# Kernel optimization log

Measured on AMD Instinct MI355X. Metric: run time of the kernel, lower is better.

Reference implementation:

```python
import jax, jax.numpy as jnp
import numpy as np

N, L, IN_DIM, H, E = 16, 4096, 32, 1, 512
D = H * E  # d_model
FF = E     # feed_forward_dimensions = embed_dim
EPS_ATTN = 1e-6
EPS_LN = 1e-5


def _ln(x, g, b):
    mu = jnp.mean(x, axis=-1, keepdims=True)
    var = jnp.mean(jnp.square(x - mu), axis=-1, keepdims=True)
    return (x - mu) * jax.lax.rsqrt(var + EPS_LN) * g + b


def setup_inputs() -> dict:
    key = jax.random.key(0)
    ks = jax.random.split(key, 16)
    s = 0.02
    inp = {
        "x": jax.random.normal(ks[0], (N, L, IN_DIM), dtype=jnp.float32),
        "w_in": jax.random.normal(ks[1], (D, IN_DIM), dtype=jnp.float32) * s,
        "b_in": jnp.zeros((D,), jnp.float32),
        "wq": jax.random.normal(ks[2], (H * E, D), dtype=jnp.float32) * s,
        "bq": jnp.zeros((H * E,), jnp.float32),
        "wk": jax.random.normal(ks[3], (H * E, D), dtype=jnp.float32) * s,
        "bk": jnp.zeros((H * E,), jnp.float32),
        "wv": jax.random.normal(ks[4], (H * E, D), dtype=jnp.float32) * s,
        "bv": jnp.zeros((H * E,), jnp.float32),
        "wo": jax.random.normal(ks[5], (D, H * E), dtype=jnp.float32) * s,
        "bo": jnp.zeros((D,), jnp.float32),
        "g1": jnp.ones((D,), jnp.float32),
        "b1": jnp.zeros((D,), jnp.float32),
        "w_ff1": jax.random.normal(ks[6], (FF, D), dtype=jnp.float32) * s,
        "b_ff1": jnp.zeros((FF,), jnp.float32),
        "w_ff2": jax.random.normal(ks[7], (D, FF), dtype=jnp.float32) * s,
        "b_ff2": jnp.zeros((D,), jnp.float32),
        "g2": jnp.ones((D,), jnp.float32),
        "b2": jnp.zeros((D,), jnp.float32),
        "gf": jnp.ones((D,), jnp.float32),
        "bf": jnp.zeros((D,), jnp.float32),
        "w_fc": jax.random.normal(ks[8], (1, D), dtype=jnp.float32) * s,
        "b_fc": jnp.zeros((1,), jnp.float32),
    }
    return inp


def reference(x, w_in, b_in, wq, bq, wk, bk, wv, bv, wo, bo, g1, b1,
              w_ff1, b_ff1, w_ff2, b_ff2, g2, b2, gf, bf, w_fc, b_fc):
    # input projection
    h = x @ w_in.T + b_in  # [N,L,D]
    # attention layer: q/k/v projections, split heads
    q = (h @ wq.T + bq).reshape(N, L, H, E)
    k = (h @ wk.T + bk).reshape(N, L, H, E)
    v = (h @ wv.T + bv).reshape(N, L, H, E)
    # linear attention: elu+1 feature map, non-causal aggregation
    Q = jax.nn.elu(q) + 1.0
    K = jax.nn.elu(k) + 1.0
    KV = jnp.einsum("nshd,nshm->nhdm", K, v)          # [N,H,E,E]
    Z = 1.0 / (jnp.einsum("nlhd,nhd->nlh", Q, K.sum(axis=1)) + EPS_ATTN)
    attn = jnp.einsum("nlhd,nhdm,nlh->nlhm", Q, KV, Z)  # [N,L,H,E]
    attn = attn.reshape(N, L, H * E) @ wo.T + bo
    # post-norm transformer encoder layer (dropout=0)
    h = _ln(h + attn, g1, b1)
    y = jax.nn.relu(h @ w_ff1.T + b_ff1) @ w_ff2.T + b_ff2
    h = _ln(h + y, g2, b2)
    # final encoder normalization
    h = _ln(h, gf, bf)
    out = h @ w_fc.T + b_fc  # [N,L,1]
    return out[:, 0, 0]
```

## Files before the change

### kernel.cpp

```cpp
#include <hip/hip_runtime.h>
#include <hip/hip_bf16.h>

typedef unsigned short u16;
typedef __attribute__((ext_vector_type(8))) unsigned short ushort8;
typedef __attribute__((ext_vector_type(8))) __bf16 bf16x8;
typedef __attribute__((ext_vector_type(4))) float f32x4;

#define NB 16
#define SEQ 4096
#define DIM 512
#define INDIM 32
#define NTOK (NB * SEQ)
#define WBM 128
#define NTILE (NTOK / WBM)

static __device__ __forceinline__ u16 f2bf(float f) {
    union { float f; unsigned u; } x; x.f = f;
    unsigned r = (x.u + 0x7FFFu + ((x.u >> 16) & 1u)) >> 16;
    return (u16)r;
}
static __device__ __forceinline__ float bf2f(u16 b) {
    union { unsigned u; float f; } x; x.u = ((unsigned)b) << 16;
    return x.f;
}

__device__ __forceinline__ float dot32(const float* __restrict__ w, const float* v) {
    const float4* a = (const float4*)w;
    float acc = 0.f;
    #pragma unroll
    for (int i = 0; i < 8; ++i) {
        float4 p = a[i];
        acc += p.x * v[4*i] + p.y * v[4*i+1] + p.z * v[4*i+2] + p.w * v[4*i+3];
    }
    return acc;
}

__global__ __launch_bounds__(256) void k_p1(
    const float* __restrict__ wq, const float* __restrict__ wk, const float* __restrict__ wv,
    const float* __restrict__ wo, const float* __restrict__ w_in, const float* __restrict__ b_in,
    const float* __restrict__ bq, const float* __restrict__ bk, const float* __restrict__ bv,
    const float* __restrict__ bo, const float* __restrict__ g1, const float* __restrict__ b1,
    const float* __restrict__ wff1, const float* __restrict__ wff2,
    float* __restrict__ wq2, float* __restrict__ bq2,
    u16* __restrict__ wk2b, float* __restrict__ bk2,
    float* __restrict__ wv2, float* __restrict__ wvb,
    float* __restrict__ wf1x, float* __restrict__ wf1c,
    float* __restrict__ wg1, float* __restrict__ wb1, float* __restrict__ bb,
    u16* __restrict__ woT, u16* __restrict__ wff1g1T, u16* __restrict__ wff2T) {
    __shared__ float smem[64 * 65];
    int bid = blockIdx.x, tid = threadIdx.x;

    if (bid < 1536) {
        int mat = bid >> 9, e = bid & 511;
        int kc = tid >> 5, j = tid & 31;
        const float* A = (mat == 0 ? wq : (mat == 1 ? wk : wv)) + (long)e * DIM;
        float acc = 0.f, accb = 0.f;
        int d0 = kc * 64;
        #pragma unroll 8
        for (int i = 0; i < 64; ++i) {
            float a = A[d0 + i];
            acc  += a * w_in[(d0 + i) * INDIM + j];
            accb += a * b_in[d0 + i];
        }
        float* sA = smem;
        float* sS = smem + 256;
        sA[kc * 32 + j] = acc;
        if (j == 0) sS[kc] = accb;
        __syncthreads();
        if (tid < 32) {
            float s = 0.f;
            #pragma unroll
            for (int i = 0; i < 8; ++i) s += sA[i * 32 + tid];
            if (mat == 0) wq2[e * INDIM + tid] = s;
            else if (mat == 1) wk2b[e * INDIM + tid] = f2bf(s);
            else wv2[e * INDIM + tid] = s;
        } else if (tid == 32) {
            float s = 0.f;
            #pragma unroll
            for (int i = 0; i < 8; ++i) s += sS[i];
            if (mat == 0) bq2[e] = bq[e] + s;
            else if (mat == 1) bk2[e] = bk[e] + s;
            else wvb[e] = s + bv[e];
        }
    } else if (bid < 2048) {
        int e = bid - 1536;
        int kc = tid >> 5, j = tid & 31;
        const float* A = wff1 + (long)e * DIM;
        float accx = 0.f, accc = 0.f, accg = 0.f, accb1 = 0.f;
        int d0 = kc * 64;
        #pragma unroll 4
        for (int i = 0; i < 64; ++i) {
            int d = d0 + i;
            float a = A[d], g = g1[d], ag = a * g;
            accx  += ag * w_in[d * INDIM + j];
            accc  += ag * (b_in[d] + bo[d]);
            accg  += ag;
            accb1 += a * b1[d];
        }
        float* sA = smem;
        float* s0 = smem + 256;
        float* s1p = smem + 264;
        float* s2 = smem + 272;
        sA[kc * 32 + j] = accx;
        if (j == 0) { s0[kc] = accc; s1p[kc] = accg; s2[kc] = accb1; }
        __syncthreads();
        if (tid < 32) {
            float s = 0.f;
            #pragma unroll
            for (int i = 0; i < 8; ++i) s += sA[i * 32 + tid];
            wf1x[e * INDIM + tid] = s;
        } else if (tid == 32) {
            float s = 0.f;
            #pragma unroll
            for (int i = 0; i < 8; ++i) s += s0[i];
            wf1c[e] = s;
        } else if (tid == 33) {
            float s = 0.f;
            #pragma unroll
            for (int i = 0; i < 8; ++i) s += s1p[i];
            wg1[e] = s;
        } else if (tid == 34) {
            float s = 0.f;
            #pragma unroll
            for (int i = 0; i < 8; ++i) s += s2[i];
            wb1[e] = s;
        } else if (tid == 35) {
            bb[e] = b_in[e] + bo[e];
        }
    } else {
        int t = bid - 2048;
        int m = t >> 6;
        int tt = t & 63;
        int r = tt >> 3, c = tt & 7;
        const float* M = (m == 0) ? wo : (m == 1 ? wff1 : wff2);
        u16* MT = (m == 0) ? woT : (m == 1 ? wff1g1T : wff2T);
        float* tile = smem;
        int rr = tid >> 2, cc = (tid & 3) * 16;
        const float* src = M + (long)(r * 64 + rr) * DIM + c * 64 + cc;
        #pragma unroll
        for (int i = 0; i < 4; ++i) {
            float4 v = *(const float4*)(src + i * 4);
            tile[rr * 65 + cc + i * 4 + 0] = v.x;
            tile[rr * 65 + cc + i * 4 + 1] = v.y;
            tile[rr * 65 + cc + i * 4 + 2] = v.z;
            tile[rr * 65 + cc + i * 4 + 3] = v.w;
        }
        __syncthreads();
        int orr = tid >> 2, occ = (tid & 3) * 16;
        float gk = (m == 1) ? g1[c * 64 + orr] : 1.f;
        u16 ob[16];
        #pragma unroll
        for (int i = 0; i < 16; ++i) ob[i] = f2bf(tile[(occ + i) * 65 + orr] * gk);
        u16* dst = MT + (long)(c * 64 + orr) * DIM + r * 64 + occ;
        *(ushort8*)dst = *(ushort8*)ob;
        *(ushort8*)(dst + 8) = *(ushort8*)(ob + 8);
    }
}

__global__ __launch_bounds__(256) void k_w(
    const float* __restrict__ x,
    const float* __restrict__ wq2, const float* __restrict__ bq2,
    const u16* __restrict__ wk2b, const float* __restrict__ bk2,
    float* __restrict__ xup, float* __restrict__ zdp) {
    __shared__ u16 sB[DIM * 40];
    __shared__ float s_q0[DIM];
    __shared__ float sw[WBM];
    __shared__ float sxu8[8][32];
    __shared__ float szz[8];
    __shared__ float sx0[INDIM];
    int tid = threadIdx.x;
    int tt = blockIdx.x;
    int lane = tid & 63, wid = tid >> 6;
    long tbase = (long)tt * WBM;
    int batch = (int)(tbase >> 12);

    #pragma unroll
    for (int pp = 0; pp < 8; ++pp) {
        int f = (pp * 256 + tid) * 8;
        int row = f >> 5, colc = f & 31;
        ushort8 v = *(const ushort8*)(wk2b + f);
        *(ushort8*)(sB + row * 40 + colc) = v;
    }
    if (tid < INDIM) sx0[tid] = x[(long)batch * SEQ * INDIM + tid];
    __syncthreads();
    #pragma unroll
    for (int rep = 0; rep < 2; ++rep) {
        int e = tid + rep * 256;
        float a = bq2[e] + dot32(wq2 + e * INDIM, sx0);
        s_q0[e] = (a > 0.f) ? (a + 1.f) : __expf(a);
    }

    int col = lane & 15;
    int koff = (lane >> 4) * 8;
    bf16x8 fa[2];
    #pragma unroll
    for (int mi = 0; mi < 2; ++mi) {
        const float* xr = x + (tbase + wid * 32 + mi * 16 + col) * INDIM + koff;
        float4 a0 = *(const float4*)(xr);
        float4 a1 = *(const float4*)(xr + 4);
        u16 tmp[8] = { f2bf(a0.x), f2bf(a0.y), f2bf(a0.z), f2bf(a0.w),
                       f2bf(a1.x), f2bf(a1.y), f2bf(a1.z), f2bf(a1.w) };
        fa[mi] = *(bf16x8*)tmp;
    }
    __syncthreads();

    float q0v[32], bkv[32];
    #pragma unroll
    for (int ni = 0; ni < 32; ++ni) {
        q0v[ni] = s_q0[ni * 16 + col];
        bkv[ni] = bk2[ni * 16 + col];
    }

    f32x4 zero = {0.f, 0.f, 0.f, 0.f};
    float wpart[2][4] = {};
    #pragma unroll
    for (int nc = 0; nc < 4; ++nc) {
        bf16x8 fb[8];
        #pragma unroll
        for (int nj = 0; nj < 8; ++nj) {
            int row = (nc * 8 + nj) * 16 + col;
            fb[nj] = *(const bf16x8*)(sB + row * 40 + koff);
        }
        #pragma unroll
        for (int mi = 0; mi < 2; ++mi) {
            #pragma unroll
            for (int nj = 0; nj < 8; ++nj) {
                f32x4 acc = __builtin_amdgcn_mfma_f32_16x16x32_bf16(fa[mi], fb[nj], zero, 0, 0, 0);
                int ni = nc * 8 + nj;
                #pragma unroll
                for (int r = 0; r < 4; ++r) {
                    float v = acc[r] + bkv[ni];
                    v = (v > 0.f) ? (v + 1.f) : __expf(v);
                    wpart[mi][r] += v * q0v[ni];
                }
            }
        }
    }
    #pragma unroll
    for (int mi = 0; mi < 2; ++mi) {
        #pragma unroll
        for (int r = 0; r < 4; ++r) {
            float s = wpart[mi][r];
            s += __shfl_xor(s, 1, 64); s += __shfl_xor(s, 2, 64);
            s += __shfl_xor(s, 4, 64); s += __shfl_xor(s, 8, 64);
            if (col == 0) sw[wid * 32 + mi * 16 + (lane >> 4) * 4 + r] = s;
        }
    }
    __syncthreads();
    {
        int j = tid & 31, g = tid >> 5;
        float a = 0.f, z = 0.f;
        for (int tl = g; tl < WBM; tl += 8) {
            float wv_ = sw[tl];
            a += wv_ * x[(tbase + tl) * INDIM + j];
            if (j == 0) z += wv_;
        }
        sxu8[g][j] = a;
        if (j == 0) szz[g] = z;
    }
    __syncthreads();
    if (tid < 32) {
        float a = 0.f;
        #pragma unroll
        for (int g = 0; g < 8; ++g) a += sxu8[g][tid];
        xup[tt * INDIM + tid] = a;
    } else if (tid == 32) {
        float z = 0.f;
        #pragma unroll
        for (int g = 0; g < 8; ++g) z += szz[g];
        zdp[tt] = z;
    }
}

__device__ __forceinline__ void reduce2_512(float a, float b, int tid, float* l16,
                                            float& oa, float& ob) {
    #pragma unroll
    for (int off = 1; off < 64; off <<= 1) {
        a += __shfl_xor(a, off, 64);
        b += __shfl_xor(b, off, 64);
    }
    int w = tid >> 6;
    if ((tid & 63) == 0) { l16[w] = a; l16[8 + w] = b; }
    __syncthreads();
    float ra = 0.f, rb = 0.f;
    #pragma unroll
    for (int i = 0; i < 8; ++i) { ra += l16[i]; rb += l16[8 + i]; }
    oa = ra; ob = rb;
    __syncthreads();
}

__device__ __forceinline__ float gemv512(const u16* __restrict__ MT,
                                         const float* __restrict__ vec,
                                         float* __restrict__ spart,
                                         int tid, int d) {
    int kc = tid >> 6, dg = tid & 63;
    float ps[8] = {};
    const u16* base = MT + (long)(kc * 64) * DIM + dg * 8;
    #pragma unroll 8
    for (int k8 = 0; k8 < 64; ++k8) {
        ushort8 w8 = *(const ushort8*)(base + (long)k8 * DIM);
        float fk = vec[kc * 64 + k8];
        #pragma unroll
        for (int j = 0; j < 8; ++j) ps[j] += bf2f(w8[j]) * fk;
    }
    #pragma unroll
    for (int j = 0; j < 8; ++j) spart[kc * DIM + dg * 8 + j] = ps[j];
    __syncthreads();
    float acc = 0.f;
    #pragma unroll
    for (int i = 0; i < 8; ++i) acc += spart[i * DIM + d];
    return acc;
}

__global__ __launch_bounds__(512) void k_final(
    const float* __restrict__ x, const float* __restrict__ w_in,
    const float* __restrict__ wv2, const float* __restrict__ wvb,
    const float* __restrict__ bb,
    const float* __restrict__ wf1x, const float* __restrict__ wf1c,
    const float* __restrict__ wg1, const float* __restrict__ wb1,
    const float* __restrict__ g1, const float* __restrict__ b1,
    const float* __restrict__ bff1, const float* __restrict__ bff2,
    const u16* __restrict__ woT, const u16* __restrict__ wff1g1T,
    const u16* __restrict__ wff2T,
    const float* __restrict__ g2, const float* __restrict__ b2,
    const float* __restrict__ gf, const float* __restrict__ bfv,
    const float* __restrict__ wfc, const float* __restrict__ bfc,
    const float* __restrict__ xup, const float* __restrict__ zdp,
    float* __restrict__ out) {
    __shared__ float sx0[INDIM], sxu[INDIM];
    __shared__ float sv[DIM];
    __shared__ float sf[DIM];
    __shared__ float spart[8 * DIM];
    __shared__ float l16[16];
    __shared__ float szd;
    int n = blockIdx.x, tid = threadIdx.x, d = tid;
    if (tid < INDIM) {
        float a = 0.f;
        #pragma unroll 8
        for (int slot = 0; slot < 32; ++slot)
            a += xup[(n * 32 + slot) * INDIM + tid];
        sxu[tid] = a;
        sx0[tid] = x[(long)n * SEQ * INDIM + tid];
    } else if (tid == 32) {
        float z = 0.f;
        #pragma unroll 8
        for (int slot = 0; slot < 32; ++slot) z += zdp[n * 32 + slot];
        szd = z;
    }
    __syncthreads();
    float zd = szd;
    float Z = 1.f / (zd + 1e-6f);
    float zz = zd * Z;

    float u2d = dot32(wv2 + d * INDIM, sxu);
    sv[d] = Z * u2d + zz * wvb[d];
    __syncthreads();

    float o_d = gemv512(woT, sv, spart, tid, d);

    float rd = bb[d] + dot32(w_in + d * INDIM, sx0) + o_d;
    sv[d] = o_d;
    float sum, sumsq;
    reduce2_512(rd, rd * rd, tid, l16, sum, sumsq);
    float mu1 = sum * (1.f / DIM);
    float s1 = rsqrtf(sumsq * (1.f / DIM) - mu1 * mu1 + 1e-5f);
    float r1 = (rd - mu1) * s1 * g1[d] + b1[d];

    float W_d = gemv512(wff1g1T, sv, spart, tid, d);
    float G = dot32(wf1x + d * INDIM, sx0) + W_d + wf1c[d];
    float fp = s1 * (G - mu1 * wg1[d]) + wb1[d] + bff1[d];
    __syncthreads();
    sf[d] = fmaxf(fp, 0.f);
    __syncthreads();

    float yacc = gemv512(wff2T, sf, spart, tid, d);
    float y = r1 + bff2[d] + yacc;

    reduce2_512(y, y * y, tid, l16, sum, sumsq);
    float mu2 = sum * (1.f / DIM);
    float inv2 = rsqrtf(sumsq * (1.f / DIM) - mu2 * mu2 + 1e-5f);
    float h2 = (y - mu2) * inv2 * g2[d] + b2[d];

    reduce2_512(h2, h2 * h2, tid, l16, sum, sumsq);
    float mu3 = sum * (1.f / DIM);
    float inv3 = rsqrtf(sumsq * (1.f / DIM) - mu3 * mu3 + 1e-5f);
    float h3 = (h2 - mu3) * inv3 * gf[d] + bfv[d];

    float pfc = wfc[d] * h3;
    float dummy;
    reduce2_512(pfc, 0.f, tid, l16, sum, dummy);
    if (tid == 0) out[n] = sum + bfc[0];
}

extern "C" void kernel_launch(void* const* d_in, const int* in_sizes, int n_in,
                              void* d_out, int out_size, void* d_ws, size_t ws_size,
                              hipStream_t stream) {
    const float* x    = (const float*)d_in[0];
    const float* w_in = (const float*)d_in[1];
    const float* b_in = (const float*)d_in[2];
    const float* wq   = (const float*)d_in[3];
    const float* bq   = (const float*)d_in[4];
    const float* wk   = (const float*)d_in[5];
    const float* bk   = (const float*)d_in[6];
    const float* wv   = (const float*)d_in[7];
    const float* bv   = (const float*)d_in[8];
    const float* wo   = (const float*)d_in[9];
    const float* bo   = (const float*)d_in[10];
    const float* g1   = (const float*)d_in[11];
    const float* b1   = (const float*)d_in[12];
    const float* wff1 = (const float*)d_in[13];
    const float* bff1 = (const float*)d_in[14];
    const float* wff2 = (const float*)d_in[15];
    const float* bff2 = (const float*)d_in[16];
    const float* g2   = (const float*)d_in[17];
    const float* b2   = (const float*)d_in[18];
    const float* gf   = (const float*)d_in[19];
    const float* bf   = (const float*)d_in[20];
    const float* wfc  = (const float*)d_in[21];
    const float* bfc  = (const float*)d_in[22];

    char* ws = (char*)d_ws;
    float* wq2     = (float*)(ws + 0);
    float* bq2     = (float*)(ws + 65536);
    u16*   wk2b    = (u16*)  (ws + 67584);
    float* bk2     = (float*)(ws + 100352);
    float* wv2     = (float*)(ws + 102400);
    float* wvb     = (float*)(ws + 167936);
    float* bb      = (float*)(ws + 169984);
    float* wf1x    = (float*)(ws + 172032);
    float* wf1c    = (float*)(ws + 237568);
    float* wg1     = (float*)(ws + 239616);
    float* wb1     = (float*)(ws + 241664);
    u16*   woT     = (u16*)  (ws + 243712);
    u16*   wff1g1T = (u16*)  (ws + 767872);
    u16*   wff2T   = (u16*)  (ws + 1292160);
    float* xup     = (float*)(ws + 1816448);
    float* zdp     = (float*)(ws + 1881984);

    k_p1<<<2240, 256, 0, stream>>>(wq, wk, wv, wo, w_in, b_in, bq, bk, bv, bo,
                                   g1, b1, wff1, wff2,
                                   wq2, bq2, wk2b, bk2, wv2, wvb,
                                   wf1x, wf1c, wg1, wb1, bb,
                                   woT, wff1g1T, wff2T);
    k_w<<<NTILE, 256, 0, stream>>>(x, wq2, bq2, wk2b, bk2, xup, zdp);
    k_final<<<NB, 512, 0, stream>>>(x, w_in, wv2, wvb, bb, wf1x, wf1c, wg1, wb1,
                                    g1, b1, bff1, bff2, woT, wff1g1T, wff2T,
                                    g2, b2, gf, bf, wfc, bfc, xup, zdp,
                                    (float*)d_out);
}
```

Measured before the change: 71.32 us.

## Fuse final per-batch epilogue into tile kernel via last-block atomic ticket

```diff
diff --git a/kernel.cpp b/kernel.cpp
--- a/kernel.cpp
+++ b/kernel.cpp
@@ -35,32 +35,43 @@
     return acc;
 }
 
-__global__ __launch_bounds__(256) void k_p1(
-    const float* __restrict__ wq, const float* __restrict__ wk, const float* __restrict__ wv,
-    const float* __restrict__ wo, const float* __restrict__ w_in, const float* __restrict__ b_in,
-    const float* __restrict__ bq, const float* __restrict__ bk, const float* __restrict__ bv,
-    const float* __restrict__ bo, const float* __restrict__ g1, const float* __restrict__ b1,
-    const float* __restrict__ wff1, const float* __restrict__ wff2,
-    float* __restrict__ wq2, float* __restrict__ bq2,
-    u16* __restrict__ wk2b, float* __restrict__ bk2,
-    float* __restrict__ wv2, float* __restrict__ wvb,
-    float* __restrict__ wf1x, float* __restrict__ wf1c,
-    float* __restrict__ wg1, float* __restrict__ wb1, float* __restrict__ bb,
-    u16* __restrict__ woT, u16* __restrict__ wff1g1T, u16* __restrict__ wff2T) {
+__device__ __forceinline__ float dot512(const float* __restrict__ w, const float* v) {
+    const float4* a = (const float4*)w;
+    float acc = 0.f;
+    #pragma unroll 4
+    for (int j = 0; j < 128; ++j) {
+        float4 p = a[j];
+        acc += p.x * v[4*j] + p.y * v[4*j+1] + p.z * v[4*j+2] + p.w * v[4*j+3];
+    }
+    return acc;
+}
+
+struct P {
+    const float *x, *w_in, *b_in, *wq, *bq, *wk, *bk, *wv, *bv, *wo, *bo;
+    const float *g1, *b1, *wff1, *bff1, *wff2, *bff2, *g2, *b2, *gf, *bfv, *wfc, *bfc;
+    u16 *wk2b; float *bk2, *wv2, *wvb;
+    float *bb, *wf1x, *wf1c, *wg1, *wb1;
+    u16 *woT, *wff1g1T, *wff2T;
+    float *q0, *xup, *zdp;
+    int *cnt;
+    float *out;
+};
+
+__global__ __launch_bounds__(256) void k_p1(P p) {
     __shared__ float smem[64 * 65];
     int bid = blockIdx.x, tid = threadIdx.x;
 
-    if (bid < 1536) {
+    if (bid < 1024) {
         int mat = bid >> 9, e = bid & 511;
         int kc = tid >> 5, j = tid & 31;
-        const float* A = (mat == 0 ? wq : (mat == 1 ? wk : wv)) + (long)e * DIM;
+        const float* A = (mat == 0 ? p.wk : p.wv) + (long)e * DIM;
         float acc = 0.f, accb = 0.f;
         int d0 = kc * 64;
         #pragma unroll 8
         for (int i = 0; i < 64; ++i) {
             float a = A[d0 + i];
-            acc  += a * w_in[(d0 + i) * INDIM + j];
-            accb += a * b_in[d0 + i];
+            acc  += a * p.w_in[(d0 + i) * INDIM + j];
+            accb += a * p.b_in[d0 + i];
         }
         float* sA = smem;
         float* sS = smem + 256;
@@ -71,31 +82,29 @@
             float s = 0.f;
             #pragma unroll
             for (int i = 0; i < 8; ++i) s += sA[i * 32 + tid];
-            if (mat == 0) wq2[e * INDIM + tid] = s;
-            else if (mat == 1) wk2b[e * INDIM + tid] = f2bf(s);
-            else wv2[e * INDIM + tid] = s;
+            if (mat == 0) p.wk2b[e * INDIM + tid] = f2bf(s);
+            else p.wv2[e * INDIM + tid] = s;
         } else if (tid == 32) {
             float s = 0.f;
             #pragma unroll
             for (int i = 0; i < 8; ++i) s += sS[i];
-            if (mat == 0) bq2[e] = bq[e] + s;
-            else if (mat == 1) bk2[e] = bk[e] + s;
-            else wvb[e] = s + bv[e];
-        }
-    } else if (bid < 2048) {
-        int e = bid - 1536;
+            if (mat == 0) p.bk2[e] = p.bk[e] + s;
+            else p.wvb[e] = s + p.bv[e];
+        }
+    } else if (bid < 1536) {
+        int e = bid - 1024;
         int kc = tid >> 5, j = tid & 31;
-        const float* A = wff1 + (long)e * DIM;
+        const float* A = p.wff1 + (long)e * DIM;
         float accx = 0.f, accc = 0.f, accg = 0.f, accb1 = 0.f;
         int d0 = kc * 64;
         #pragma unroll 4
         for (int i = 0; i < 64; ++i) {
             int d = d0 + i;
-            float a = A[d], g = g1[d], ag = a * g;
-            accx  += ag * w_in[d * INDIM + j];
-            accc  += ag * (b_in[d] + bo[d]);
+            float a = A[d], g = p.g1[d], ag = a * g;
+            accx  += ag * p.w_in[d * INDIM + j];
+            accc  += ag * (p.b_in[d] + p.bo[d]);
             accg  += ag;
-            accb1 += a * b1[d];
+            accb1 += a * p.b1[d];
         }
         float* sA = smem;
         float* s0 = smem + 256;
@@ -108,32 +117,32 @@
             float s = 0.f;
             #pragma unroll
             for (int i = 0; i < 8; ++i) s += sA[i * 32 + tid];
-            wf1x[e * INDIM + tid] = s;
+            p.wf1x[e * INDIM + tid] = s;
         } else if (tid == 32) {
             float s = 0.f;
             #pragma unroll
             for (int i = 0; i < 8; ++i) s += s0[i];
-            wf1c[e] = s;
+            p.wf1c[e] = s;
         } else if (tid == 33) {
             float s = 0.f;
             #pragma unroll
             for (int i = 0; i < 8; ++i) s += s1p[i];
-            wg1[e] = s;
+            p.wg1[e] = s;
         } else if (tid == 34) {
             float s = 0.f;
             #pragma unroll
             for (int i = 0; i < 8; ++i) s += s2[i];
-            wb1[e] = s;
+            p.wb1[e] = s;
         } else if (tid == 35) {
-            bb[e] = b_in[e] + bo[e];
-        }
-    } else {
-        int t = bid - 2048;
+            p.bb[e] = p.b_in[e] + p.bo[e];
+        }
+    } else if (bid < 1728) {
+        int t = bid - 1536;
         int m = t >> 6;
         int tt = t & 63;
         int r = tt >> 3, c = tt & 7;
-        const float* M = (m == 0) ? wo : (m == 1 ? wff1 : wff2);
-        u16* MT = (m == 0) ? woT : (m == 1 ? wff1g1T : wff2T);
+        const float* M = (m == 0) ? p.wo : (m == 1 ? p.wff1 : p.wff2);
+        u16* MT = (m == 0) ? p.woT : (m == 1 ? p.wff1g1T : p.wff2T);
         float* tile = smem;
         int rr = tid >> 2, cc = (tid & 3) * 16;
         const float* src = M + (long)(r * 64 + rr) * DIM + c * 64 + cc;
@@ -147,47 +156,175 @@
         }
         __syncthreads();
         int orr = tid >> 2, occ = (tid & 3) * 16;
-        float gk = (m == 1) ? g1[c * 64 + orr] : 1.f;
+        float gk = (m == 1) ? p.g1[c * 64 + orr] : 1.f;
         u16 ob[16];
         #pragma unroll
         for (int i = 0; i < 16; ++i) ob[i] = f2bf(tile[(occ + i) * 65 + orr] * gk);
         u16* dst = MT + (long)(c * 64 + orr) * DIM + r * 64 + occ;
         *(ushort8*)dst = *(ushort8*)ob;
         *(ushort8*)(dst + 8) = *(ushort8*)(ob + 8);
-    }
-}
-
-__global__ __launch_bounds__(256) void k_w(
-    const float* __restrict__ x,
-    const float* __restrict__ wq2, const float* __restrict__ bq2,
-    const u16* __restrict__ wk2b, const float* __restrict__ bk2,
-    float* __restrict__ xup, float* __restrict__ zdp) {
-    __shared__ u16 sB[DIM * 40];
-    __shared__ float s_q0[DIM];
-    __shared__ float sw[WBM];
-    __shared__ float sxu8[8][32];
-    __shared__ float szz[8];
-    __shared__ float sx0[INDIM];
+    } else {
+        int n = bid - 1728;
+        float* sx0 = smem;
+        float* sh = smem + 32;
+        if (tid < INDIM) sx0[tid] = p.x[(long)n * SEQ * INDIM + tid];
+        __syncthreads();
+        #pragma unroll
+        for (int rep = 0; rep < 2; ++rep) {
+            int d = tid + rep * 256;
+            sh[d] = p.b_in[d] + dot32(p.w_in + (long)d * INDIM, sx0);
+        }
+        __syncthreads();
+        #pragma unroll
+        for (int rep = 0; rep < 2; ++rep) {
+            int e = tid + rep * 256;
+            float a = p.bq[e] + dot512(p.wq + (long)e * DIM, sh);
+            p.q0[n * DIM + e] = (a > 0.f) ? (a + 1.f) : __expf(a);
+        }
+        if (tid == 0) p.cnt[n] = 0;
+    }
+}
+
+__device__ __forceinline__ void reduce2_256(float a, float b, int tid, float* l16,
+                                            float& oa, float& ob) {
+    #pragma unroll
+    for (int off = 1; off < 64; off <<= 1) {
+        a += __shfl_xor(a, off, 64);
+        b += __shfl_xor(b, off, 64);
+    }
+    int w = tid >> 6;
+    if ((tid & 63) == 0) { l16[w] = a; l16[4 + w] = b; }
+    __syncthreads();
+    oa = l16[0] + l16[1] + l16[2] + l16[3];
+    ob = l16[4] + l16[5] + l16[6] + l16[7];
+    __syncthreads();
+}
+
+__device__ __forceinline__ void gemv256(const u16* __restrict__ MT,
+                                        const float* __restrict__ vec,
+                                        float* __restrict__ spart,
+                                        int tid, float& o0, float& o1) {
+    int kc = tid >> 6, dg = tid & 63;
+    float ps[8] = {};
+    const u16* base = MT + (long)(kc * 128) * DIM + dg * 8;
+    #pragma unroll 8
+    for (int k8 = 0; k8 < 128; ++k8) {
+        ushort8 w8 = *(const ushort8*)(base + (long)k8 * DIM);
+        float fk = vec[kc * 128 + k8];
+        #pragma unroll
+        for (int j = 0; j < 8; ++j) ps[j] += bf2f(w8[j]) * fk;
+    }
+    #pragma unroll
+    for (int j = 0; j < 8; ++j) spart[kc * DIM + dg * 8 + j] = ps[j];
+    __syncthreads();
+    float a0 = 0.f, a1 = 0.f;
+    #pragma unroll
+    for (int i = 0; i < 4; ++i) {
+        a0 += spart[i * DIM + tid];
+        a1 += spart[i * DIM + tid + 256];
+    }
+    o0 = a0; o1 = a1;
+}
+
+__device__ void phaseE256(const P& p, int n, int tid, char* smem) {
+    float* sx0 = (float*)smem;
+    float* sxu = sx0 + 32;
+    float* sv  = sxu + 32;
+    float* sf  = sv + 512;
+    float* spart = sf + 512;
+    float* l16 = spart + 2048;
+    float* szd = l16 + 8;
+    if (tid < INDIM) {
+        float a = 0.f;
+        #pragma unroll 8
+        for (int slot = 0; slot < 32; ++slot)
+            a += p.xup[(n * 32 + slot) * INDIM + tid];
+        sxu[tid] = a;
+        sx0[tid] = p.x[(long)n * SEQ * INDIM + tid];
+    } else if (tid == 32) {
+        float z = 0.f;
+        #pragma unroll 8
+        for (int slot = 0; slot < 32; ++slot) z += p.zdp[n * 32 + slot];
+        szd[0] = z;
+    }
+    __syncthreads();
+    float zd = szd[0];
+    float Z = 1.f / (zd + 1e-6f);
+    float zz = zd * Z;
+    int d0 = tid, d1 = tid + 256;
+
+    sv[d0] = Z * dot32(p.wv2 + (long)d0 * INDIM, sxu) + zz * p.wvb[d0];
+    sv[d1] = Z * dot32(p.wv2 + (long)d1 * INDIM, sxu) + zz * p.wvb[d1];
+    __syncthreads();
+
+    float o0, o1;
+    gemv256(p.woT, sv, spart, tid, o0, o1);
+
+    float rd0 = p.bb[d0] + dot32(p.w_in + (long)d0 * INDIM, sx0) + o0;
+    float rd1 = p.bb[d1] + dot32(p.w_in + (long)d1 * INDIM, sx0) + o1;
+    sv[d0] = o0;
+    sv[d1] = o1;
+    float sum, sumsq;
+    reduce2_256(rd0 + rd1, rd0 * rd0 + rd1 * rd1, tid, l16, sum, sumsq);
+    float mu1 = sum * (1.f / DIM);
+    float s1 = rsqrtf(sumsq * (1.f / DIM) - mu1 * mu1 + 1e-5f);
+    float r1_0 = (rd0 - mu1) * s1 * p.g1[d0] + p.b1[d0];
+    float r1_1 = (rd1 - mu1) * s1 * p.g1[d1] + p.b1[d1];
+
+    float W0, W1;
+    gemv256(p.wff1g1T, sv, spart, tid, W0, W1);
+    float G0 = dot32(p.wf1x + (long)d0 * INDIM, sx0) + W0 + p.wf1c[d0];
+    float G1 = dot32(p.wf1x + (long)d1 * INDIM, sx0) + W1 + p.wf1c[d1];
+    float fp0 = s1 * (G0 - mu1 * p.wg1[d0]) + p.wb1[d0] + p.bff1[d0];
+    float fp1 = s1 * (G1 - mu1 * p.wg1[d1]) + p.wb1[d1] + p.bff1[d1];
+    __syncthreads();
+    sf[d0] = fmaxf(fp0, 0.f);
+    sf[d1] = fmaxf(fp1, 0.f);
+    __syncthreads();
+
+    float ya0, ya1;
+    gemv256(p.wff2T, sf, spart, tid, ya0, ya1);
+    float y0 = r1_0 + p.bff2[d0] + ya0;
+    float y1 = r1_1 + p.bff2[d1] + ya1;
+
+    reduce2_256(y0 + y1, y0 * y0 + y1 * y1, tid, l16, sum, sumsq);
+    float mu2 = sum * (1.f / DIM);
+    float inv2 = rsqrtf(sumsq * (1.f / DIM) - mu2 * mu2 + 1e-5f);
+    float h2_0 = (y0 - mu2) * inv2 * p.g2[d0] + p.b2[d0];
+    float h2_1 = (y1 - mu2) * inv2 * p.g2[d1] + p.b2[d1];
+
+    reduce2_256(h2_0 + h2_1, h2_0 * h2_0 + h2_1 * h2_1, tid, l16, sum, sumsq);
+    float mu3 = sum * (1.f / DIM);
+    float inv3 = rsqrtf(sumsq * (1.f / DIM) - mu3 * mu3 + 1e-5f);
+    float h3_0 = (h2_0 - mu3) * inv3 * p.gf[d0] + p.bfv[d0];
+    float h3_1 = (h2_1 - mu3) * inv3 * p.gf[d1] + p.bfv[d1];
+
+    float pr = p.wfc[d0] * h3_0 + p.wfc[d1] * h3_1;
+    float dummy;
+    reduce2_256(pr, 0.f, tid, l16, sum, dummy);
+    if (tid == 0) p.out[n] = sum + p.bfc[0];
+}
+
+__global__ __launch_bounds__(256) void k_wE(P p) {
+    __shared__ __align__(16) char smem[45056];
+    __shared__ int sTicket;
     int tid = threadIdx.x;
     int tt = blockIdx.x;
     int lane = tid & 63, wid = tid >> 6;
     long tbase = (long)tt * WBM;
     int batch = (int)(tbase >> 12);
 
+    u16* sB = (u16*)smem;
+    float* sw = (float*)(smem + 40960);
+    float* sxu8 = (float*)(smem + 41472);
+    float* szz = (float*)(smem + 42496);
+
     #pragma unroll
     for (int pp = 0; pp < 8; ++pp) {
         int f = (pp * 256 + tid) * 8;
         int row = f >> 5, colc = f & 31;
-        ushort8 v = *(const ushort8*)(wk2b + f);
+        ushort8 v = *(const ushort8*)(p.wk2b + f);
         *(ushort8*)(sB + row * 40 + colc) = v;
-    }
-    if (tid < INDIM) sx0[tid] = x[(long)batch * SEQ * INDIM + tid];
-    __syncthreads();
-    #pragma unroll
-    for (int rep = 0; rep < 2; ++rep) {
-        int e = tid + rep * 256;
-        float a = bq2[e] + dot32(wq2 + e * INDIM, sx0);
-        s_q0[e] = (a > 0.f) ? (a + 1.f) : __expf(a);
     }
 
     int col = lane & 15;
@@ -195,21 +332,20 @@
     bf16x8 fa[2];
     #pragma unroll
     for (int mi = 0; mi < 2; ++mi) {
-        const float* xr = x + (tbase + wid * 32 + mi * 16 + col) * INDIM + koff;
+        const float* xr = p.x + (tbase + wid * 32 + mi * 16 + col) * INDIM + koff;
         float4 a0 = *(const float4*)(xr);
         float4 a1 = *(const float4*)(xr + 4);
         u16 tmp[8] = { f2bf(a0.x), f2bf(a0.y), f2bf(a0.z), f2bf(a0.w),
                        f2bf(a1.x), f2bf(a1.y), f2bf(a1.z), f2bf(a1.w) };
         fa[mi] = *(bf16x8*)tmp;
     }
-    __syncthreads();
-
     float q0v[32], bkv[32];
     #pragma unroll
     for (int ni = 0; ni < 32; ++ni) {
-        q0v[ni] = s_q0[ni * 16 + col];
-        bkv[ni] = bk2[ni * 16 + col];
-    }
+        q0v[ni] = p.q0[batch * DIM + ni * 16 + col];
+        bkv[ni] = p.bk2[ni * 16 + col];
+    }
+    __syncthreads();
 
     f32x4 zero = {0.f, 0.f, 0.f, 0.f};
     float wpart[2][4] = {};
@@ -252,199 +388,82 @@
         float a = 0.f, z = 0.f;
         for (int tl = g; tl < WBM; tl += 8) {
             float wv_ = sw[tl];
-            a += wv_ * x[(tbase + tl) * INDIM + j];
+            a += wv_ * p.x[(tbase + tl) * INDIM + j];
             if (j == 0) z += wv_;
         }
-        sxu8[g][j] = a;
+        sxu8[g * 32 + j] = a;
         if (j == 0) szz[g] = z;
     }
     __syncthreads();
     if (tid < 32) {
         float a = 0.f;
         #pragma unroll
-        for (int g = 0; g < 8; ++g) a += sxu8[g][tid];
-        xup[tt * INDIM + tid] = a;
+        for (int g = 0; g < 8; ++g) a += sxu8[g * 32 + tid];
+        p.xup[tt * INDIM + tid] = a;
     } else if (tid == 32) {
         float z = 0.f;
         #pragma unroll
         for (int g = 0; g < 8; ++g) z += szz[g];
-        zdp[tt] = z;
-    }
-}
-
-__device__ __forceinline__ void reduce2_512(float a, float b, int tid, float* l16,
-                                            float& oa, float& ob) {
-    #pragma unroll
-    for (int off = 1; off < 64; off <<= 1) {
-        a += __shfl_xor(a, off, 64);
-        b += __shfl_xor(b, off, 64);
-    }
-    int w = tid >> 6;
-    if ((tid & 63) == 0) { l16[w] = a; l16[8 + w] = b; }
-    __syncthreads();
-    float ra = 0.f, rb = 0.f;
-    #pragma unroll
-    for (int i = 0; i < 8; ++i) { ra += l16[i]; rb += l16[8 + i]; }
-    oa = ra; ob = rb;
-    __syncthreads();
-}
-
-__device__ __forceinline__ float gemv512(const u16* __restrict__ MT,
-                                         const float* __restrict__ vec,
-                                         float* __restrict__ spart,
-                                         int tid, int d) {
-    int kc = tid >> 6, dg = tid & 63;
-    float ps[8] = {};
-    const u16* base = MT + (long)(kc * 64) * DIM + dg * 8;
-    #pragma unroll 8
-    for (int k8 = 0; k8 < 64; ++k8) {
-        ushort8 w8 = *(const ushort8*)(base + (long)k8 * DIM);
-        float fk = vec[kc * 64 + k8];
-        #pragma unroll
-        for (int j = 0; j < 8; ++j) ps[j] += bf2f(w8[j]) * fk;
-    }
-    #pragma unroll
-    for (int j = 0; j < 8; ++j) spart[kc * DIM + dg * 8 + j] = ps[j];
-    __syncthreads();
-    float acc = 0.f;
-    #pragma unroll
-    for (int i = 0; i < 8; ++i) acc += spart[i * DIM + d];
-    return acc;
-}
-
-__global__ __launch_bounds__(512) void k_final(
-    const float* __restrict__ x, const float* __restrict__ w_in,
-    const float* __restrict__ wv2, const float* __restrict__ wvb,
-    const float* __restrict__ bb,
-    const float* __restrict__ wf1x, const float* __restrict__ wf1c,
-    const float* __restrict__ wg1, const float* __restrict__ wb1,
-    const float* __restrict__ g1, const float* __restrict__ b1,
-    const float* __restrict__ bff1, const float* __restrict__ bff2,
-    const u16* __restrict__ woT, const u16* __restrict__ wff1g1T,
-    const u16* __restrict__ wff2T,
-    const float* __restrict__ g2, const float* __restrict__ b2,
-    const float* __restrict__ gf, const float* __restrict__ bfv,
-    const float* __restrict__ wfc, const float* __restrict__ bfc,
-    const float* __restrict__ xup, const float* __restrict__ zdp,
-    float* __restrict__ out) {
-    __shared__ float sx0[INDIM], sxu[INDIM];
-    __shared__ float sv[DIM];
-    __shared__ float sf[DIM];
-    __shared__ float spart[8 * DIM];
-    __shared__ float l16[16];
-    __shared__ float szd;
-    int n = blockIdx.x, tid = threadIdx.x, d = tid;
-    if (tid < INDIM) {
-        float a = 0.f;
-        #pragma unroll 8
-        for (int slot = 0; slot < 32; ++slot)
-            a += xup[(n * 32 + slot) * INDIM + tid];
-        sxu[tid] = a;
-        sx0[tid] = x[(long)n * SEQ * INDIM + tid];
-    } else if (tid == 32) {
-        float z = 0.f;
-        #pragma unroll 8
-        for (int slot = 0; slot < 32; ++slot) z += zdp[n * 32 + slot];
-        szd = z;
-    }
-    __syncthreads();
-    float zd = szd;
-    float Z = 1.f / (zd + 1e-6f);
-    float zz = zd * Z;
-
-    float u2d = dot32(wv2 + d * INDIM, sxu);
-    sv[d] = Z * u2d + zz * wvb[d];
-    __syncthreads();
-
-    float o_d = gemv512(woT, sv, spart, tid, d);
-
-    float rd = bb[d] + dot32(w_in + d * INDIM, sx0) + o_d;
-    sv[d] = o_d;
-    float sum, sumsq;
-    reduce2_512(rd, rd * rd, tid, l16, sum, sumsq);
-    float mu1 = sum * (1.f / DIM);
-    float s1 = rsqrtf(sumsq * (1.f / DIM) - mu1 * mu1 + 1e-5f);
-    float r1 = (rd - mu1) * s1 * g1[d] + b1[d];
-
-    float W_d = gemv512(wff1g1T, sv, spart, tid, d);
-    float G = dot32(wf1x + d * INDIM, sx0) + W_d + wf1c[d];
-    float fp = s1 * (G - mu1 * wg1[d]) + wb1[d] + bff1[d];
-    __syncthreads();
-    sf[d] = fmaxf(fp, 0.f);
-    __syncthreads();
-
-    float yacc = gemv512(wff2T, sf, spart, tid, d);
-    float y = r1 + bff2[d] + yacc;
-
-    reduce2_512(y, y * y, tid, l16, sum, sumsq);
-    float mu2 = sum * (1.f / DIM);
-    float inv2 = rsqrtf(sumsq * (1.f / DIM) - mu2 * mu2 + 1e-5f);
-    float h2 = (y - mu2) * inv2 * g2[d] + b2[d];
-
-    reduce2_512(h2, h2 * h2, tid, l16, sum, sumsq);
-    float mu3 = sum * (1.f / DIM);
-    float inv3 = rsqrtf(sumsq * (1.f / DIM) - mu3 * mu3 + 1e-5f);
-    float h3 = (h2 - mu3) * inv3 * gf[d] + bfv[d];
-
-    float pfc = wfc[d] * h3;
-    float dummy;
-    reduce2_512(pfc, 0.f, tid, l16, sum, dummy);
-    if (tid == 0) out[n] = sum + bfc[0];
+        p.zdp[tt] = z;
+    }
+
+    __threadfence();
+    __syncthreads();
+    if (tid == 0) sTicket = atomicAdd(&p.cnt[batch], 1);
+    __syncthreads();
+    if (sTicket == 31) {
+        __threadfence();
+        phaseE256(p, batch, tid, smem);
+    }
 }
 
 extern "C" void kernel_launch(void* const* d_in, const int* in_sizes, int n_in,
                               void* d_out, int out_size, void* d_ws, size_t ws_size,
                               hipStream_t stream) {
-    const float* x    = (const float*)d_in[0];
-    const float* w_in = (const float*)d_in[1];
-    const float* b_in = (const float*)d_in[2];
-    const float* wq   = (const float*)d_in[3];
-    const float* bq   = (const float*)d_in[4];
-    const float* wk   = (const float*)d_in[5];
-    const float* bk   = (const float*)d_in[6];
-    const float* wv   = (const float*)d_in[7];
-    const float* bv   = (const float*)d_in[8];
-    const float* wo   = (const float*)d_in[9];
-    const float* bo   = (const float*)d_in[10];
-    const float* g1   = (const float*)d_in[11];
-    const float* b1   = (const float*)d_in[12];
-    const float* wff1 = (const float*)d_in[13];
-    const float* bff1 = (const float*)d_in[14];
-    const float* wff2 = (const float*)d_in[15];
-    const float* bff2 = (const float*)d_in[16];
-    const float* g2   = (const float*)d_in[17];
-    const float* b2   = (const float*)d_in[18];
-    const float* gf   = (const float*)d_in[19];
-    const float* bf   = (const float*)d_in[20];
-    const float* wfc  = (const float*)d_in[21];
-    const float* bfc  = (const float*)d_in[22];
-
     char* ws = (char*)d_ws;
-    float* wq2     = (float*)(ws + 0);
-    float* bq2     = (float*)(ws + 65536);
-    u16*   wk2b    = (u16*)  (ws + 67584);
-    float* bk2     = (float*)(ws + 100352);
-    float* wv2     = (float*)(ws + 102400);
-    float* wvb     = (float*)(ws + 167936);
-    float* bb      = (float*)(ws + 169984);
-    float* wf1x    = (float*)(ws + 172032);
-    float* wf1c    = (float*)(ws + 237568);
-    float* wg1     = (float*)(ws + 239616);
-    float* wb1     = (float*)(ws + 241664);
-    u16*   woT     = (u16*)  (ws + 243712);
-    u16*   wff1g1T = (u16*)  (ws + 767872);
-    u16*   wff2T   = (u16*)  (ws + 1292160);
-    float* xup     = (float*)(ws + 1816448);
-    float* zdp     = (float*)(ws + 1881984);
-
-    k_p1<<<2240, 256, 0, stream>>>(wq, wk, wv, wo, w_in, b_in, bq, bk, bv, bo,
-                                   g1, b1, wff1, wff2,
-                                   wq2, bq2, wk2b, bk2, wv2, wvb,
-                                   wf1x, wf1c, wg1, wb1, bb,
-                                   woT, wff1g1T, wff2T);
-    k_w<<<NTILE, 256, 0, stream>>>(x, wq2, bq2, wk2b, bk2, xup, zdp);
-    k_final<<<NB, 512, 0, stream>>>(x, w_in, wv2, wvb, bb, wf1x, wf1c, wg1, wb1,
-                                    g1, b1, bff1, bff2, woT, wff1g1T, wff2T,
-                                    g2, b2, gf, bf, wfc, bfc, xup, zdp,
-                                    (float*)d_out);
-}
+    P p;
+    p.x    = (const float*)d_in[0];
+    p.w_in = (const float*)d_in[1];
+    p.b_in = (const float*)d_in[2];
+    p.wq   = (const float*)d_in[3];
+    p.bq   = (const float*)d_in[4];
+    p.wk   = (const float*)d_in[5];
+    p.bk   = (const float*)d_in[6];
+    p.wv   = (const float*)d_in[7];
+    p.bv   = (const float*)d_in[8];
+    p.wo   = (const float*)d_in[9];
+    p.bo   = (const float*)d_in[10];
+    p.g1   = (const float*)d_in[11];
+    p.b1   = (const float*)d_in[12];
+    p.wff1 = (const float*)d_in[13];
+    p.bff1 = (const float*)d_in[14];
+    p.wff2 = (const float*)d_in[15];
+    p.bff2 = (const float*)d_in[16];
+    p.g2   = (const float*)d_in[17];
+    p.b2   = (const float*)d_in[18];
+    p.gf   = (const float*)d_in[19];
+    p.bfv  = (const float*)d_in[20];
+    p.wfc  = (const float*)d_in[21];
+    p.bfc  = (const float*)d_in[22];
+
+    p.wk2b    = (u16*)  (ws + 0);
+    p.bk2     = (float*)(ws + 32768);
+    p.wv2     = (float*)(ws + 34816);
+    p.wvb     = (float*)(ws + 100352);
+    p.bb      = (float*)(ws + 102400);
+    p.wf1x    = (float*)(ws + 104448);
+    p.wf1c    = (float*)(ws + 169984);
+    p.wg1     = (float*)(ws + 172032);
+    p.wb1     = (float*)(ws + 174080);
+    p.woT     = (u16*)  (ws + 176128);
+    p.wff1g1T = (u16*)  (ws + 700416);
+    p.wff2T   = (u16*)  (ws + 1224704);
+    p.q0      = (float*)(ws + 1748992);
+    p.xup     = (float*)(ws + 1781760);
+    p.zdp     = (float*)(ws + 1847296);
+    p.cnt     = (int*)  (ws + 1849344);
+    p.out     = (float*)d_out;
+
+    k_p1<<<1744, 256, 0, stream>>>(p);
+    k_wE<<<NTILE, 256, 0, stream>>>(p);
+}
```

Result: slower. 139.6 us (+95.7%).
